# Performance work log

Hardware: AMD Instinct MI355X
Metric: run time of the kernel (lower is better)

Reference implementation:

```python
import jax, jax.numpy as jnp
import numpy as np
import math

DIM = 1024
N_HEAD = 16
HEAD_DIM = DIM // N_HEAD  # 64
B, T = 4, 2048


def rotate_half(x):
    # lucidrains-style interleaved rotation: (x1, x2) pairs -> (-x2, x1)
    x = x.reshape(*x.shape[:-1], -1, 2)
    x1, x2 = x[..., 0], x[..., 1]
    return jnp.stack((-x2, x1), axis=-1).reshape(*x.shape[:-2], -1)


def apply_rope(x):
    # x: [b, h, t, d]
    d = x.shape[-1]
    t = x.shape[-2]
    inv_freq = 1.0 / (10000.0 ** (jnp.arange(0, d, 2, dtype=jnp.float32) / d))  # [d/2]
    angles = jnp.arange(t, dtype=jnp.float32)[:, None] * inv_freq[None, :]      # [t, d/2]
    angles = jnp.repeat(angles, 2, axis=-1)                                     # [t, d] interleaved
    cos, sin = jnp.cos(angles), jnp.sin(angles)
    return x * cos + rotate_half(x) * sin


def setup_inputs() -> dict:
    key = jax.random.key(0)
    kx, kw1, kb1, kw2, kb2 = jax.random.split(key, 5)
    x = jax.random.normal(kx, (B, T, DIM), dtype=jnp.float32)
    mask = jnp.tril(jnp.ones((T, T), dtype=jnp.int32))  # causal
    s = 0.02
    qkv_w = jax.random.normal(kw1, (DIM, 3 * DIM), dtype=jnp.float32) * s
    qkv_b = jax.random.normal(kb1, (3 * DIM,), dtype=jnp.float32) * s
    out_w = jax.random.normal(kw2, (DIM, DIM), dtype=jnp.float32) * s
    out_b = jax.random.normal(kb2, (DIM,), dtype=jnp.float32) * s
    return {"x": x, "mask": mask, "qkv_w": qkv_w, "qkv_b": qkv_b,
            "out_w": out_w, "out_b": out_b}


def reference(x, mask, qkv_w, qkv_b, out_w, out_b):
    b, t, _ = x.shape
    qkv = x @ qkv_w + qkv_b                       # [b, t, 3*dim]
    q, k, v = jnp.split(qkv, 3, axis=-1)
    def to_heads(z):
        return z.reshape(b, t, N_HEAD, HEAD_DIM).transpose(0, 2, 1, 3)  # [b,h,t,d]
    q, k, v = to_heads(q), to_heads(k), to_heads(v)
    q = apply_rope(q)
    k = apply_rope(k)
    scores = jnp.einsum('bhqd,bhkd->bhqk', q, k) / math.sqrt(HEAD_DIM)
    scores = jnp.where(mask[None, None, :, :] == 0, -jnp.inf, scores)
    attn = jax.nn.softmax(scores, axis=-1)        # dropout = identity (eval)
    out = jnp.einsum('bhqk,bhkd->bhqd', attn, v)  # [b,h,t,d]
    out = out.transpose(0, 2, 1, 3).reshape(b, t, DIM)
    return out @ out_w + out_b
```

## Files before the change

### kernel.cpp

```cpp
#include <hip/hip_runtime.h>

typedef __bf16 bf16_t;
typedef __bf16 bf16x8 __attribute__((ext_vector_type(8)));
typedef float  f32x4  __attribute__((ext_vector_type(4)));
typedef float  f32x16 __attribute__((ext_vector_type(16)));
typedef unsigned u32x4 __attribute__((ext_vector_type(4)));

#define DIMM  1024
#define NHEAD 16
#define HDIM  64
#define BATCH 4
#define SEQ   2048
#define MROWS (BATCH*SEQ)

#define AQB   128
#define AKV   64
#define NP    (SEQ/AQB)
#define SKS   72
#define LOG2E 1.44269504088896f

__device__ __forceinline__ void gload_lds16(const bf16_t* g, bf16_t* l) {
  __builtin_amdgcn_global_load_lds(
      (const __attribute__((address_space(1))) void*)g,
      (__attribute__((address_space(3))) void*)l, 16, 0, 0);
}

__device__ __forceinline__ unsigned short f2bu(float f) {
  bf16_t b = (bf16_t)f;
  return __builtin_bit_cast(unsigned short, b);
}
__device__ __forceinline__ float bu2f(unsigned short u) {
  return __uint_as_float(((unsigned)u) << 16);
}
__device__ __forceinline__ unsigned packbf(float a, float b) {
  return (unsigned)f2bu(a) | ((unsigned)f2bu(b) << 16);
}
__device__ __forceinline__ float fexp2(float x) {
  float r; asm("v_exp_f32 %0, %1" : "=v"(r) : "v"(x)); return r;
}

__global__ void k_convert(const float* __restrict__ in, bf16_t* __restrict__ out, int n4) {
  int i = blockIdx.x * blockDim.x + threadIdx.x;
  if (i >= n4) return;
  float4 v = reinterpret_cast<const float4*>(in)[i];
  ushort4 o;
  o.x = f2bu(v.x); o.y = f2bu(v.y); o.z = f2bu(v.z); o.w = f2bu(v.w);
  reinterpret_cast<ushort4*>(out)[i] = o;
}

__global__ void k_transpose_convert(const float* __restrict__ in, bf16_t* __restrict__ out,
                                    int R, int C) {
  __shared__ float tile[32][33];
  int cb = blockIdx.x * 32, rb = blockIdx.y * 32;
  int tx = threadIdx.x, ty = threadIdx.y;
  #pragma unroll
  for (int i = 0; i < 4; ++i)
    tile[ty + i*8][tx] = in[(size_t)(rb + ty + i*8) * C + cb + tx];
  __syncthreads();
  #pragma unroll
  for (int i = 0; i < 4; ++i)
    out[(size_t)(cb + ty + i*8) * R + rb + tx] = (bf16_t)tile[tx][ty + i*8];
}

__global__ void k_rope_table(float* __restrict__ cosT, float* __restrict__ sinT) {
  int id = blockIdx.x * blockDim.x + threadIdx.x;
  if (id >= SEQ * 32) return;
  int t = id >> 5, i = id & 31;
  double ang = (double)t * pow(10000.0, -(double)i / 32.0);
  cosT[id] = (float)cos(ang);
  sinT[id] = (float)sin(ang);
}

__global__ void k_rope(bf16_t* __restrict__ Q, bf16_t* __restrict__ Kb,
                       const float* __restrict__ cosT, const float* __restrict__ sinT) {
  int id = blockIdx.x * blockDim.x + threadIdx.x;
  if (id >= 64 * SEQ * 32) return;
  int i = id & 31;
  int t = (id >> 5) & (SEQ - 1);
  float c = cosT[(t << 5) + i], s = sinT[(t << 5) + i];
  unsigned* Qu = reinterpret_cast<unsigned*>(Q);
  unsigned* Ku = reinterpret_cast<unsigned*>(Kb);
  const float qs = 0.125f * LOG2E;
  {
    unsigned u = Qu[id];
    float x1 = bu2f((unsigned short)(u & 0xffffu));
    float x2 = bu2f((unsigned short)(u >> 16));
    Qu[id] = packbf((x1 * c - x2 * s) * qs, (x2 * c + x1 * s) * qs);
  }
  {
    unsigned u = Ku[id];
    float x1 = bu2f((unsigned short)(u & 0xffffu));
    float x2 = bu2f((unsigned short)(u >> 16));
    Ku[id] = packbf(x1 * c - x2 * s, x2 * c + x1 * s);
  }
}

template<int MODE>
__global__ __launch_bounds__(256) void k_gemm(
    const bf16_t* __restrict__ A, const bf16_t* __restrict__ BT,
    const float* __restrict__ bias,
    bf16_t* __restrict__ q, bf16_t* __restrict__ k, bf16_t* __restrict__ v,
    float* __restrict__ outf, int M, int N, int K)
{
  __shared__ bf16_t sA[128 * 32];
  __shared__ bf16_t sB[128 * 32];
  const int tid = threadIdx.x;
  const int w = tid >> 6, lane = tid & 63;
  const int wr = w >> 1, wc = w & 1;
  const int l15 = lane & 15, l4 = lane >> 4;

  int nwg = gridDim.x * gridDim.y;
  int id  = blockIdx.y * gridDim.x + blockIdx.x;
  int cpx = nwg >> 3;
  int sid = (id & 7) * cpx + (id >> 3);
  int bx = sid % gridDim.x, by = sid / gridDim.x;

  const int rowA0 = by * 128;
  const int colB0 = bx * 128;

  f32x4 acc[4][4] = {};

  const int nkt = K >> 5;
  for (int kt = 0; kt < nkt; ++kt) {
    __syncthreads();
    #pragma unroll
    for (int i = 0; i < 2; ++i) {
      int c = i * 256 + w * 64 + lane;
      int row = c >> 2, k8 = (c & 3) * 8;
      gload_lds16(A  + (size_t)(rowA0 + row) * K + kt * 32 + k8, sA + (i * 256 + w * 64) * 8);
      gload_lds16(BT + (size_t)(colB0 + row) * K + kt * 32 + k8, sB + (i * 256 + w * 64) * 8);
    }
    asm volatile("s_waitcnt vmcnt(0)" ::: "memory");
    __syncthreads();
    bf16x8 af[4], bfr[4];
    #pragma unroll
    for (int mi = 0; mi < 4; ++mi)
      af[mi] = *reinterpret_cast<const bf16x8*>(sA + (wr * 64 + mi * 16 + l15) * 32 + l4 * 8);
    #pragma unroll
    for (int ni = 0; ni < 4; ++ni)
      bfr[ni] = *reinterpret_cast<const bf16x8*>(sB + (wc * 64 + ni * 16 + l15) * 32 + l4 * 8);
    #pragma unroll
    for (int mi = 0; mi < 4; ++mi)
      #pragma unroll
      for (int ni = 0; ni < 4; ++ni)
        acc[mi][ni] = __builtin_amdgcn_mfma_f32_16x16x32_bf16(af[mi], bfr[ni], acc[mi][ni], 0, 0, 0);
  }

  #pragma unroll
  for (int mi = 0; mi < 4; ++mi) {
    #pragma unroll
    for (int ni = 0; ni < 4; ++ni) {
      int n = colB0 + wc * 64 + ni * 16 + l15;
      float bs = bias[n];
      #pragma unroll
      for (int r = 0; r < 4; ++r) {
        int m = rowA0 + wr * 64 + mi * 16 + l4 * 4 + r;
        float val = acc[mi][ni][r] + bs;
        if (MODE == 0) {
          int which = n >> 10, hd = n & 1023;
          int h = hd >> 6, d = hd & 63;
          int b = m >> 11, t = m & 2047;
          bf16_t* dst = (which == 0) ? q : (which == 1) ? k : v;
          dst[((size_t)(b * NHEAD + h) * SEQ + t) * HDIM + d] = (bf16_t)val;
        } else {
          outf[(size_t)m * N + n] = val;
        }
      }
    }
  }
}

__global__ __launch_bounds__(256, 2) void k_attn(
    const bf16_t* __restrict__ Q, const bf16_t* __restrict__ Kb,
    const bf16_t* __restrict__ Vb, bf16_t* __restrict__ O)
{
  __shared__ bf16_t sK[2][64 * SKS];
  __shared__ bf16_t sV[2][64 * SKS];

  const int tid = threadIdx.x;
  const int w = tid >> 6, lane = tid & 63;
  const int l31 = lane & 31, hi = lane >> 5;

  const int id = blockIdx.x;
  const int j4 = id >> 8;
  const int k4 = (id >> 6) & 3;
  const int bh = id & 63;
  const int qblk = (j4 == 0) ? 15 - 2 * k4
                 : (j4 == 1) ? 2 * k4
                 : (j4 == 2) ? 14 - 2 * k4
                 :             2 * k4 + 1;

  const size_t hbase = (size_t)bh * SEQ * HDIM;
  const int b = bh >> 4, h = bh & 15;
  const int srow = tid >> 3, sslot = tid & 7;

  const int qbase = qblk * AQB + 32 * w;
  const int nt = 2 * qblk + 2;

  bf16x8 qf[4];
  #pragma unroll
  for (int kt = 0; kt < 4; ++kt)
    qf[kt] = *reinterpret_cast<const bf16x8*>(
        Q + hbase + (size_t)(qbase + l31) * HDIM + kt * 16 + hi * 8);
  asm volatile("s_waitcnt vmcnt(0)" ::: "memory");
  asm volatile("" : "+v"(qf[0]), "+v"(qf[1]), "+v"(qf[2]), "+v"(qf[3]));

  u32x4 kr[2], vr[2];
  auto issue = [&](int t) {
    const bf16_t* kp = Kb + hbase + (size_t)(t * AKV + srow) * HDIM + sslot * 8;
    const bf16_t* vp = Vb + hbase + (size_t)(t * AKV + srow) * HDIM + sslot * 8;
    asm volatile("global_load_dwordx4 %0, %1, off" : "=v"(kr[0]) : "v"(kp));
    asm volatile("global_load_dwordx4 %0, %1, off" : "=v"(kr[1]) : "v"(kp + 32 * HDIM));
    asm volatile("global_load_dwordx4 %0, %1, off" : "=v"(vr[0]) : "v"(vp));
    asm volatile("global_load_dwordx4 %0, %1, off" : "=v"(vr[1]) : "v"(vp + 32 * HDIM));
  };
  auto stage = [&](int nb) {
    #pragma unroll
    for (int cc = 0; cc < 2; ++cc) {
      int row = srow + 32 * cc;
      *reinterpret_cast<u32x4*>(&sK[nb][row * SKS + ((sslot ^ (row >> 3)) << 3)]) = kr[cc];
      bf16x8 vv = __builtin_bit_cast(bf16x8, vr[cc]);
      #pragma unroll
      for (int j = 0; j < 8; ++j) {
        int d = sslot * 8 + j;
        sV[nb][d * SKS + (((row >> 3) ^ sslot) << 3) + (row & 7)] = vv[j];
      }
    }
  };

  float mrun = -1e30f, lrun = 0.f;
  f32x16 accO[2] = {};

  issue(0);
  asm volatile("s_waitcnt vmcnt(0)" ::: "memory");
  stage(0);
  issue(1);
  asm volatile("s_waitcnt lgkmcnt(0)" ::: "memory");
  __builtin_amdgcn_s_barrier();
  asm volatile("" ::: "memory");

  for (int t = 0; t < nt; ++t) {
    const int c = t & 1;
    if (t + 1 < nt) {
      asm volatile("s_waitcnt vmcnt(0)" ::: "memory");
      stage(c ^ 1);
      if (t + 2 < nt) issue(t + 2);
    }
    const bool masked = (t * AKV + AKV - 1 > qbase);
    #pragma unroll
    for (int sub = 0; sub < 2; ++sub) {
      f32x16 sc = {};
      __builtin_amdgcn_s_setprio(1);
      #pragma unroll
      for (int kt = 0; kt < 4; ++kt) {
        int krow = 32 * sub + l31;
        bf16x8 kf = *reinterpret_cast<const bf16x8*>(
            &sK[c][krow * SKS + (((2 * kt + hi) ^ (krow >> 3)) << 3)]);
        sc = __builtin_amdgcn_mfma_f32_32x32x16_bf16(kf, qf[kt], sc, 0, 0, 0);
      }
      __builtin_amdgcn_s_setprio(0);

      float p[16];
      const int qa = qbase + l31;
      const int kb0 = t * AKV + 32 * sub + 4 * hi;
      #pragma unroll
      for (int r = 0; r < 16; ++r) {
        float s = sc[r];
        if (masked) {
          int kvi = kb0 + (r & 3) + 8 * (r >> 2);
          if (kvi > qa) s = -1e30f;
        }
        p[r] = s;
      }
      float m0 = fmaxf(fmaxf(p[0],  p[1]),  p[2]);
      float m1 = fmaxf(fmaxf(p[3],  p[4]),  p[5]);
      float m2 = fmaxf(fmaxf(p[6],  p[7]),  p[8]);
      float m3 = fmaxf(fmaxf(p[9],  p[10]), p[11]);
      float m4 = fmaxf(fmaxf(p[12], p[13]), p[14]);
      float mt = fmaxf(fmaxf(fmaxf(m0, m1), fmaxf(m2, m3)), fmaxf(m4, p[15]));
      mt = fmaxf(mt, __shfl_xor(mt, 32));
      if (!__all(mt <= mrun + 11.54f)) {
        float mnew = fmaxf(mrun, mt);
        float scl = fexp2(mrun - mnew);
        mrun = mnew;
        lrun *= scl;
        #pragma unroll
        for (int i = 0; i < 16; ++i) { accO[0][i] *= scl; accO[1][i] *= scl; }
      }
      float rs = 0.f;
      #pragma unroll
      for (int r = 0; r < 16; ++r) { p[r] = fexp2(p[r] - mrun); rs += p[r]; }
      lrun += rs + __shfl_xor(rs, 32);

      bf16x8 pf[2];
      #pragma unroll
      for (int kt = 0; kt < 2; ++kt) {
        unsigned P01 = packbf(p[8*kt+0], p[8*kt+1]);
        unsigned P23 = packbf(p[8*kt+2], p[8*kt+3]);
        unsigned P45 = packbf(p[8*kt+4], p[8*kt+5]);
        unsigned P67 = packbf(p[8*kt+6], p[8*kt+7]);
        unsigned ra = __shfl_xor(hi == 0 ? P45 : P01, 32);
        unsigned rb = __shfl_xor(hi == 0 ? P67 : P23, 32);
        unsigned dw0 = hi == 0 ? P01 : ra;
        unsigned dw1 = hi == 0 ? P23 : rb;
        unsigned dw2 = hi == 0 ? ra : P45;
        unsigned dw3 = hi == 0 ? rb : P67;
        pf[kt] = __builtin_bit_cast(bf16x8, (u32x4){dw0, dw1, dw2, dw3});
      }

      __builtin_amdgcn_s_setprio(1);
      #pragma unroll
      for (int dt = 0; dt < 2; ++dt) {
        #pragma unroll
        for (int kt = 0; kt < 2; ++kt) {
          int vrow = 32 * dt + l31;
          bf16x8 vf = *reinterpret_cast<const bf16x8*>(
              &sV[c][vrow * SKS + (((4 * sub + 2 * kt + hi) ^ (vrow >> 3)) << 3)]);
          accO[dt] = __builtin_amdgcn_mfma_f32_32x32x16_bf16(vf, pf[kt], accO[dt], 0, 0, 0);
        }
      }
      __builtin_amdgcn_s_setprio(0);
    }
    asm volatile("s_waitcnt lgkmcnt(0)" ::: "memory");
    __builtin_amdgcn_s_barrier();
    asm volatile("" ::: "memory");
  }

  bf16_t* sOw = &sK[0][0] + w * (32 * SKS);
  float inv = 1.f / lrun;
  #pragma unroll
  for (int dt = 0; dt < 2; ++dt)
    #pragma unroll
    for (int r = 0; r < 16; ++r) {
      int d = 32 * dt + (r & 3) + 8 * (r >> 2) + 4 * hi;
      sOw[l31 * SKS + (d ^ ((l31 >> 3) << 3))] = (bf16_t)(accO[dt][r] * inv);
    }
  #pragma unroll
  for (int i = 0; i < 4; ++i) {
    int qr = 8 * i + (lane >> 3);
    int ch = lane & 7;
    bf16x8 vvv = *reinterpret_cast<const bf16x8*>(
        &sOw[qr * SKS + ((ch ^ (qr >> 3)) << 3)]);
    *reinterpret_cast<bf16x8*>(
        O + ((size_t)(b * SEQ + qbase + qr)) * DIMM + h * HDIM + ch * 8) = vvv;
  }
}

extern "C" void kernel_launch(void* const* d_in, const int* in_sizes, int n_in,
                              void* d_out, int out_size, void* d_ws, size_t ws_size,
                              hipStream_t stream) {
  const float* x     = (const float*)d_in[0];
  const float* qkv_w = (const float*)d_in[2];
  const float* qkv_b = (const float*)d_in[3];
  const float* out_w = (const float*)d_in[4];
  const float* out_b = (const float*)d_in[5];
  float* out = (float*)d_out;

  char* ws = (char*)d_ws;
  size_t off = 0;
  auto alloc = [&](size_t bytes) {
    char* p = ws + off;
    off += (bytes + 255) & ~(size_t)255;
    return (void*)p;
  };
  bf16_t* Xb    = (bf16_t*)alloc((size_t)MROWS * DIMM * 2);
  bf16_t* WqkvT = (bf16_t*)alloc((size_t)3 * DIMM * DIMM * 2);
  bf16_t* WoutT = (bf16_t*)alloc((size_t)DIMM * DIMM * 2);
  bf16_t* Qh    = (bf16_t*)alloc((size_t)64 * SEQ * HDIM * 2);
  bf16_t* Kh    = (bf16_t*)alloc((size_t)64 * SEQ * HDIM * 2);
  bf16_t* Vh    = (bf16_t*)alloc((size_t)64 * SEQ * HDIM * 2);
  bf16_t* AO    = (bf16_t*)alloc((size_t)MROWS * DIMM * 2);
  float*  cosT  = (float*)alloc((size_t)SEQ * 32 * 4);
  float*  sinT  = (float*)alloc((size_t)SEQ * 32 * 4);

  k_convert<<<(MROWS * DIMM / 4 + 255) / 256, 256, 0, stream>>>(x, Xb, MROWS * DIMM / 4);
  k_transpose_convert<<<dim3(3 * DIMM / 32, DIMM / 32), dim3(32, 8), 0, stream>>>(qkv_w, WqkvT, DIMM, 3 * DIMM);
  k_transpose_convert<<<dim3(DIMM / 32, DIMM / 32), dim3(32, 8), 0, stream>>>(out_w, WoutT, DIMM, DIMM);
  k_rope_table<<<(SEQ * 32 + 255) / 256, 256, 0, stream>>>(cosT, sinT);

  k_gemm<0><<<dim3(3 * DIMM / 128, MROWS / 128), 256, 0, stream>>>(
      Xb, WqkvT, qkv_b, Qh, Kh, Vh, nullptr, MROWS, 3 * DIMM, DIMM);

  k_rope<<<(64 * SEQ * 32 + 255) / 256, 256, 0, stream>>>(Qh, Kh, cosT, sinT);

  k_attn<<<dim3(NP * 64), 256, 0, stream>>>(Qh, Kh, Vh, AO);

  k_gemm<1><<<dim3(DIMM / 128, MROWS / 128), 256, 0, stream>>>(
      AO, WoutT, out_b, nullptr, nullptr, nullptr, out, MROWS, DIMM, DIMM);
}
```

Before: 212.2 us.

## Rewrite QKV GEMM with 256x256 tiles, double-buffered async LDS loads and swizzle

```diff
diff --git a/kernel.cpp b/kernel.cpp
--- a/kernel.cpp
+++ b/kernel.cpp
@@ -95,12 +95,123 @@
   }
 }
 
-template<int MODE>
-__global__ __launch_bounds__(256) void k_gemm(
+__global__ __launch_bounds__(512, 2) void k_gemm0(
     const bf16_t* __restrict__ A, const bf16_t* __restrict__ BT,
     const float* __restrict__ bias,
-    bf16_t* __restrict__ q, bf16_t* __restrict__ k, bf16_t* __restrict__ v,
-    float* __restrict__ outf, int M, int N, int K)
+    bf16_t* __restrict__ q, bf16_t* __restrict__ k, bf16_t* __restrict__ v)
+{
+  __shared__ bf16_t sA[2][2][128 * 64];
+  __shared__ bf16_t sB[2][2][128 * 64];
+
+  const int tid = threadIdx.x;
+  const int w = tid >> 6;
+  const int lane = tid & 63;
+  const int wm = w >> 2, wn = w & 3;
+  const int l15 = lane & 15, l4 = lane >> 4;
+
+  int nwg = gridDim.x * gridDim.y;
+  int id  = blockIdx.y * gridDim.x + blockIdx.x;
+  int cpx = nwg >> 3;
+  int sid = (id & 7) * cpx + (id >> 3);
+  int bx = sid % gridDim.x, by = sid / gridDim.x;
+  const int rowA0 = by * 256, colB0 = bx * 256;
+
+  f32x4 acc[8][4] = {};
+  bf16x8 bf_[4];
+
+  auto stage = [&](int tile, int part) {
+    if (tile >= 16) return;
+    const int kh = part >> 1;
+    const bool isB = part & 1;
+    const bf16_t* src = isB ? BT : A;
+    const int r0 = isB ? colB0 : rowA0;
+    bf16_t* dst = (isB ? &sB[0][0][0] : &sA[0][0][0]) + ((tile & 1) * 2 + kh) * (128 * 64);
+    #pragma unroll
+    for (int call = 0; call < 2; ++call) {
+      int n = call * 512 + tid;
+      int R = n >> 3, slot = n & 7;
+      int sp = slot ^ (R & 7);
+      int row = R * 2 + (sp >> 2);
+      gload_lds16(src + (size_t)(r0 + row) * 1024 + tile * 64 + kh * 32 + (sp & 3) * 8,
+                  dst + n * 8);
+    }
+  };
+
+  auto rdA = [&](int bc, int kh, int mfa) -> bf16x8 {
+    int row = wm * 128 + mfa * 16 + l15;
+    int R = row >> 1;
+    int slot = (((row & 1) << 2) | l4) ^ (R & 7);
+    return *reinterpret_cast<const bf16x8*>(&sA[bc][kh][R * 64 + slot * 8]);
+  };
+  auto rdB = [&](int bc, int kh, int nf) -> bf16x8 {
+    int row = wn * 64 + nf * 16 + l15;
+    int R = row >> 1;
+    int slot = (((row & 1) << 2) | l4) ^ (R & 7);
+    return *reinterpret_cast<const bf16x8*>(&sB[bc][kh][R * 64 + slot * 8]);
+  };
+
+  auto phase = [&](int bc, int kh, int mh, int stile, int spart, int wait_n) {
+    bf16x8 af[4];
+    if (mh == 0) {
+      #pragma unroll
+      for (int nf = 0; nf < 4; ++nf) bf_[nf] = rdB(bc, kh, nf);
+    }
+    #pragma unroll
+    for (int mf = 0; mf < 4; ++mf) af[mf] = rdA(bc, kh, mh * 4 + mf);
+    stage(stile, spart);
+    if (wait_n == 4)      asm volatile("s_waitcnt vmcnt(4)" ::: "memory");
+    else if (wait_n == 0) asm volatile("s_waitcnt vmcnt(0)" ::: "memory");
+    __builtin_amdgcn_s_barrier();
+    __builtin_amdgcn_s_setprio(1);
+    #pragma unroll
+    for (int mf = 0; mf < 4; ++mf)
+      #pragma unroll
+      for (int nf = 0; nf < 4; ++nf)
+        acc[mh * 4 + mf][nf] = __builtin_amdgcn_mfma_f32_16x16x32_bf16(
+            af[mf], bf_[nf], acc[mh * 4 + mf][nf], 0, 0, 0);
+    __builtin_amdgcn_s_setprio(0);
+    __builtin_amdgcn_s_barrier();
+  };
+
+  stage(0, 0); stage(0, 1); stage(0, 2); stage(0, 3);
+  stage(1, 0); stage(1, 1);
+  asm volatile("s_waitcnt vmcnt(4)" ::: "memory");
+  __builtin_amdgcn_s_barrier();
+
+  for (int i = 0; i < 8; ++i) {
+    const int t0 = 2 * i, t1 = 2 * i + 1;
+    phase(0, 0, 0, t1,     2, -1);
+    phase(0, 0, 1, t1,     3, -1);
+    phase(0, 1, 0, t0 + 2, 0, -1);
+    phase(0, 1, 1, t0 + 2, 1, (t0 + 2 < 16) ? 4 : 0);
+    phase(1, 0, 0, t0 + 2, 2, -1);
+    phase(1, 0, 1, t0 + 2, 3, -1);
+    phase(1, 1, 0, t0 + 3, 0, -1);
+    phase(1, 1, 1, t0 + 3, 1, (t0 + 3 < 16) ? 4 : 0);
+  }
+
+  #pragma unroll
+  for (int mfa = 0; mfa < 8; ++mfa) {
+    #pragma unroll
+    for (int nf = 0; nf < 4; ++nf) {
+      int n = colB0 + wn * 64 + nf * 16 + l15;
+      float bs = bias[n];
+      int which = n >> 10, hd = n & 1023;
+      int h = hd >> 6, d = hd & 63;
+      bf16_t* dst = (which == 0) ? q : (which == 1) ? k : v;
+      #pragma unroll
+      for (int r = 0; r < 4; ++r) {
+        int m = rowA0 + wm * 128 + mfa * 16 + l4 * 4 + r;
+        int b = m >> 11, t = m & 2047;
+        dst[((size_t)(b * NHEAD + h) * SEQ + t) * HDIM + d] = (bf16_t)(acc[mfa][nf][r] + bs);
+      }
+    }
+  }
+}
+
+__global__ __launch_bounds__(256) void k_gemm1(
+    const bf16_t* __restrict__ A, const bf16_t* __restrict__ BT,
+    const float* __restrict__ bias, float* __restrict__ outf, int M, int N, int K)
 {
   __shared__ bf16_t sA[128 * 32];
   __shared__ bf16_t sB[128 * 32];
@@ -155,16 +266,7 @@
       #pragma unroll
       for (int r = 0; r < 4; ++r) {
         int m = rowA0 + wr * 64 + mi * 16 + l4 * 4 + r;
-        float val = acc[mi][ni][r] + bs;
-        if (MODE == 0) {
-          int which = n >> 10, hd = n & 1023;
-          int h = hd >> 6, d = hd & 63;
-          int b = m >> 11, t = m & 2047;
-          bf16_t* dst = (which == 0) ? q : (which == 1) ? k : v;
-          dst[((size_t)(b * NHEAD + h) * SEQ + t) * HDIM + d] = (bf16_t)val;
-        } else {
-          outf[(size_t)m * N + n] = val;
-        }
+        outf[(size_t)m * N + n] = acc[mi][ni][r] + bs;
       }
     }
   }
@@ -378,13 +480,13 @@
   k_transpose_convert<<<dim3(DIMM / 32, DIMM / 32), dim3(32, 8), 0, stream>>>(out_w, WoutT, DIMM, DIMM);
   k_rope_table<<<(SEQ * 32 + 255) / 256, 256, 0, stream>>>(cosT, sinT);
 
-  k_gemm<0><<<dim3(3 * DIMM / 128, MROWS / 128), 256, 0, stream>>>(
-      Xb, WqkvT, qkv_b, Qh, Kh, Vh, nullptr, MROWS, 3 * DIMM, DIMM);
+  k_gemm0<<<dim3(3 * DIMM / 256, MROWS / 256), 512, 0, stream>>>(
+      Xb, WqkvT, qkv_b, Qh, Kh, Vh);
 
   k_rope<<<(64 * SEQ * 32 + 255) / 256, 256, 0, stream>>>(Qh, Kh, cosT, sinT);
 
   k_attn<<<dim3(NP * 64), 256, 0, stream>>>(Qh, Kh, Vh, AO);
 
-  k_gemm<1><<<dim3(DIMM / 128, MROWS / 128), 256, 0, stream>>>(
-      AO, WoutT, out_b, nullptr, nullptr, nullptr, out, MROWS, DIMM, DIMM);
-}
+  k_gemm1<<<dim3(DIMM / 128, MROWS / 128), 256, 0, stream>>>(
+      AO, WoutT, out_b, out, MROWS, DIMM, DIMM);
+}
```

After: 203.6 us. 1.04x faster.
